# Performance work log

Hardware: AMD Instinct MI355X
Metric: run time of the kernel (lower is better)

The kernel has to match this reference:

```python
import jax, jax.numpy as jnp
import numpy as np

SMOOTH = 0.6


def setup_inputs() -> dict:
    key = jax.random.key(0)
    k1, k2 = jax.random.split(key)
    B, C, H, W = 32, 2, 1024, 1024
    outputs = jax.random.normal(k1, (B, C, H, W), dtype=jnp.float32)
    targets = jax.random.randint(k2, (B, H, W), 0, C, dtype=jnp.int64)
    return {"outputs": outputs, "targets": targets}


def reference(outputs, targets):
    B, C, H, W = outputs.shape
    # Per-sample bincount of class labels: counts [B, C]
    b_idx = jnp.arange(B)[:, None, None]
    counts = jnp.zeros((B, C), jnp.float32).at[b_idx, targets].add(1.0)
    # Instance weights: inverse-frequency, blended toward the per-sample mean
    weights = 1.0 - counts / counts.sum(axis=1, keepdims=True)
    weights = weights * (1.0 - SMOOTH) + weights.mean(axis=1, keepdims=True) * SMOOTH
    # Weighted cross-entropy per sample (F.cross_entropy mean reduction with
    # class weights divides by the sum of per-pixel weights)
    logp = jax.nn.log_softmax(outputs, axis=1)               # [B, C, H, W]
    nll = -jnp.take_along_axis(logp, targets[:, None], axis=1)[:, 0]  # [B, H, W]
    w_t = jnp.take_along_axis(weights, targets.reshape(B, -1), axis=1)
    w_t = w_t.reshape(B, H, W)                               # [B, H, W]
    per_sample = (w_t * nll).sum(axis=(1, 2)) / w_t.sum(axis=(1, 2))  # [B]
    return per_sample.mean()
```

## Files before the change

kernel.cpp:

```cpp
#include <hip/hip_runtime.h>

#define BB 32
#define HW (1024 * 1024)
#define BLOCKS_PER_SAMPLE 64
#define THREADS 256

__global__ __launch_bounds__(THREADS) void iwce_main(
    const float* __restrict__ outputs,
    const int* __restrict__ targets,
    float* __restrict__ s_all,
    float* __restrict__ s_one,
    unsigned int* __restrict__ c_one) {
    const int b = blockIdx.y;
    const int chunk = blockIdx.x;
    const int tid = threadIdx.x;

    const float* __restrict__ x0p = outputs + (size_t)b * 2 * HW;
    const float* __restrict__ x1p = x0p + HW;
    const int* __restrict__ tp = targets + (size_t)b * HW;

    const int pixelsPerBlock = HW / BLOCKS_PER_SAMPLE;
    const int base = chunk * pixelsPerBlock;
    const int iters = pixelsPerBlock / (THREADS * 4);

    float acc_all = 0.f;
    float acc_one = 0.f;
    unsigned int cnt_one = 0u;

#pragma unroll 4
    for (int j = 0; j < iters; ++j) {
        const int idx = base + (j * THREADS + tid) * 4;
        const float4 x0 = *reinterpret_cast<const float4*>(x0p + idx);
        const float4 x1 = *reinterpret_cast<const float4*>(x1p + idx);
        const int4 t = *reinterpret_cast<const int4*>(tp + idx);

        {
            const float a = x0.x, c = x1.x;
            const float m = fmaxf(a, c);
            const float nll = m + __logf(1.0f + __expf(-fabsf(a - c))) - (t.x ? c : a);
            acc_all += nll;
            if (t.x) { acc_one += nll; cnt_one++; }
        }
        {
            const float a = x0.y, c = x1.y;
            const float m = fmaxf(a, c);
            const float nll = m + __logf(1.0f + __expf(-fabsf(a - c))) - (t.y ? c : a);
            acc_all += nll;
            if (t.y) { acc_one += nll; cnt_one++; }
        }
        {
            const float a = x0.z, c = x1.z;
            const float m = fmaxf(a, c);
            const float nll = m + __logf(1.0f + __expf(-fabsf(a - c))) - (t.z ? c : a);
            acc_all += nll;
            if (t.z) { acc_one += nll; cnt_one++; }
        }
        {
            const float a = x0.w, c = x1.w;
            const float m = fmaxf(a, c);
            const float nll = m + __logf(1.0f + __expf(-fabsf(a - c))) - (t.w ? c : a);
            acc_all += nll;
            if (t.w) { acc_one += nll; cnt_one++; }
        }
    }

    const int lane = tid & 63;
    const int wid = tid >> 6;
#pragma unroll
    for (int off = 32; off; off >>= 1) {
        acc_all += __shfl_down(acc_all, off, 64);
        acc_one += __shfl_down(acc_one, off, 64);
        cnt_one += __shfl_down(cnt_one, off, 64);
    }
    __shared__ float sA[THREADS / 64], sO[THREADS / 64];
    __shared__ unsigned int sC[THREADS / 64];
    if (lane == 0) { sA[wid] = acc_all; sO[wid] = acc_one; sC[wid] = cnt_one; }
    __syncthreads();
    if (tid == 0) {
        float a = 0.f, o = 0.f; unsigned int c = 0u;
#pragma unroll
        for (int w = 0; w < THREADS / 64; ++w) { a += sA[w]; o += sO[w]; c += sC[w]; }
        atomicAdd(&s_all[b], a);
        atomicAdd(&s_one[b], o);
        atomicAdd(&c_one[b], c);
    }
}

__global__ __launch_bounds__(64) void iwce_final(
    const float* __restrict__ s_all,
    const float* __restrict__ s_one,
    const unsigned int* __restrict__ c_one,
    float* __restrict__ out) {
    const int lane = threadIdx.x;
    float v = 0.f;
    if (lane < BB) {
        const float sa = s_all[lane];
        const float s1 = s_one[lane];
        const float n1 = (float)c_one[lane];
        const float n0 = (float)HW - n1;
        const float invHW = 1.0f / (float)HW;
        const float w0 = (n1 * invHW) * 0.4f + 0.3f;
        const float w1 = (n0 * invHW) * 0.4f + 0.3f;
        const float num = w0 * (sa - s1) + w1 * s1;
        const float den = w0 * n0 + w1 * n1;
        v = num / den;
    }
#pragma unroll
    for (int off = 32; off; off >>= 1) v += __shfl_down(v, off, 64);
    if (lane == 0) out[0] = v * (1.0f / (float)BB);
}

extern "C" void kernel_launch(void* const* d_in, const int* in_sizes, int n_in,
                              void* d_out, int out_size, void* d_ws, size_t ws_size,
                              hipStream_t stream) {
    const float* outputs = (const float*)d_in[0];
    const int* targets = (const int*)d_in[1];
    float* out = (float*)d_out;

    float* s_all = (float*)d_ws;
    float* s_one = s_all + BB;
    unsigned int* c_one = (unsigned int*)(s_one + BB);

    hipMemsetAsync(d_ws, 0, (2 * BB) * sizeof(float) + BB * sizeof(unsigned int), stream);

    iwce_main<<<dim3(BLOCKS_PER_SAMPLE, BB), THREADS, 0, stream>>>(
        outputs, targets, s_all, s_one, c_one);
    iwce_final<<<1, 64, 0, stream>>>(s_all, s_one, c_one, out);
}
```

Baseline: 440.5 us.

## Use nontemporal loads, branchless accumulation, and per-block partials instead of atomics

Switches the streaming loads to nontemporal builtins, makes the per-pixel accumulation branchless, and replaces the global atomics with per-block partial sums that the final kernel reduces deterministically. This removes the memset launch and atomic contention. Counts are now accumulated as floats, which stays exact here because they never exceed 2^24.

```diff
diff --git a/kernel.cpp b/kernel.cpp
--- a/kernel.cpp
+++ b/kernel.cpp
@@ -3,17 +3,22 @@
 #define BB 32
 #define HW (1024 * 1024)
 #define BLOCKS_PER_SAMPLE 64
+#define NPART (BB * BLOCKS_PER_SAMPLE)
 #define THREADS 256
+
+typedef float v4f __attribute__((ext_vector_type(4)));
+typedef int v4i __attribute__((ext_vector_type(4)));
 
 __global__ __launch_bounds__(THREADS) void iwce_main(
     const float* __restrict__ outputs,
     const int* __restrict__ targets,
-    float* __restrict__ s_all,
-    float* __restrict__ s_one,
-    unsigned int* __restrict__ c_one) {
+    float* __restrict__ pA,
+    float* __restrict__ pO,
+    float* __restrict__ pC) {
     const int b = blockIdx.y;
     const int chunk = blockIdx.x;
     const int tid = threadIdx.x;
+    const int g = b * BLOCKS_PER_SAMPLE + chunk;
 
     const float* __restrict__ x0p = outputs + (size_t)b * 2 * HW;
     const float* __restrict__ x1p = x0p + HW;
@@ -25,89 +30,85 @@
 
     float acc_all = 0.f;
     float acc_one = 0.f;
-    unsigned int cnt_one = 0u;
+    int cnt_one = 0;
 
 #pragma unroll 4
     for (int j = 0; j < iters; ++j) {
         const int idx = base + (j * THREADS + tid) * 4;
-        const float4 x0 = *reinterpret_cast<const float4*>(x0p + idx);
-        const float4 x1 = *reinterpret_cast<const float4*>(x1p + idx);
-        const int4 t = *reinterpret_cast<const int4*>(tp + idx);
+        const v4f x0 = __builtin_nontemporal_load(reinterpret_cast<const v4f*>(x0p + idx));
+        const v4f x1 = __builtin_nontemporal_load(reinterpret_cast<const v4f*>(x1p + idx));
+        const v4i t = __builtin_nontemporal_load(reinterpret_cast<const v4i*>(tp + idx));
 
-        {
-            const float a = x0.x, c = x1.x;
+#pragma unroll
+        for (int k = 0; k < 4; ++k) {
+            const float a = x0[k], c = x1[k];
             const float m = fmaxf(a, c);
-            const float nll = m + __logf(1.0f + __expf(-fabsf(a - c))) - (t.x ? c : a);
+            const float nll = m + __logf(1.0f + __expf(-fabsf(a - c))) - (t[k] ? c : a);
             acc_all += nll;
-            if (t.x) { acc_one += nll; cnt_one++; }
-        }
-        {
-            const float a = x0.y, c = x1.y;
-            const float m = fmaxf(a, c);
-            const float nll = m + __logf(1.0f + __expf(-fabsf(a - c))) - (t.y ? c : a);
-            acc_all += nll;
-            if (t.y) { acc_one += nll; cnt_one++; }
-        }
-        {
-            const float a = x0.z, c = x1.z;
-            const float m = fmaxf(a, c);
-            const float nll = m + __logf(1.0f + __expf(-fabsf(a - c))) - (t.z ? c : a);
-            acc_all += nll;
-            if (t.z) { acc_one += nll; cnt_one++; }
-        }
-        {
-            const float a = x0.w, c = x1.w;
-            const float m = fmaxf(a, c);
-            const float nll = m + __logf(1.0f + __expf(-fabsf(a - c))) - (t.w ? c : a);
-            acc_all += nll;
-            if (t.w) { acc_one += nll; cnt_one++; }
+            acc_one += t[k] ? nll : 0.0f;
+            cnt_one += t[k];
         }
     }
 
     const int lane = tid & 63;
     const int wid = tid >> 6;
+    float acc_cnt = (float)cnt_one;
 #pragma unroll
     for (int off = 32; off; off >>= 1) {
         acc_all += __shfl_down(acc_all, off, 64);
         acc_one += __shfl_down(acc_one, off, 64);
-        cnt_one += __shfl_down(cnt_one, off, 64);
+        acc_cnt += __shfl_down(acc_cnt, off, 64);
     }
-    __shared__ float sA[THREADS / 64], sO[THREADS / 64];
-    __shared__ unsigned int sC[THREADS / 64];
-    if (lane == 0) { sA[wid] = acc_all; sO[wid] = acc_one; sC[wid] = cnt_one; }
+    __shared__ float sA[THREADS / 64], sO[THREADS / 64], sC[THREADS / 64];
+    if (lane == 0) { sA[wid] = acc_all; sO[wid] = acc_one; sC[wid] = acc_cnt; }
     __syncthreads();
     if (tid == 0) {
-        float a = 0.f, o = 0.f; unsigned int c = 0u;
+        float a = 0.f, o = 0.f, c = 0.f;
 #pragma unroll
         for (int w = 0; w < THREADS / 64; ++w) { a += sA[w]; o += sO[w]; c += sC[w]; }
-        atomicAdd(&s_all[b], a);
-        atomicAdd(&s_one[b], o);
-        atomicAdd(&c_one[b], c);
+        pA[g] = a; pO[g] = o; pC[g] = c;
     }
 }
 
-__global__ __launch_bounds__(64) void iwce_final(
-    const float* __restrict__ s_all,
-    const float* __restrict__ s_one,
-    const unsigned int* __restrict__ c_one,
+__global__ __launch_bounds__(1024) void iwce_final(
+    const float* __restrict__ pA,
+    const float* __restrict__ pO,
+    const float* __restrict__ pC,
     float* __restrict__ out) {
-    const int lane = threadIdx.x;
-    float v = 0.f;
-    if (lane < BB) {
-        const float sa = s_all[lane];
-        const float s1 = s_one[lane];
-        const float n1 = (float)c_one[lane];
-        const float n0 = (float)HW - n1;
-        const float invHW = 1.0f / (float)HW;
-        const float w0 = (n1 * invHW) * 0.4f + 0.3f;
-        const float w1 = (n0 * invHW) * 0.4f + 0.3f;
-        const float num = w0 * (sa - s1) + w1 * s1;
-        const float den = w0 * n0 + w1 * n1;
-        v = num / den;
+    const int tid = threadIdx.x;
+    const int wave = tid >> 6;
+    const int lane = tid & 63;
+    __shared__ float sv[BB];
+
+#pragma unroll
+    for (int s = 0; s < 2; ++s) {
+        const int b = wave + s * 16;
+        const int idx = b * BLOCKS_PER_SAMPLE + lane;
+        float a = pA[idx], o = pO[idx], c = pC[idx];
+#pragma unroll
+        for (int off = 32; off; off >>= 1) {
+            a += __shfl_down(a, off, 64);
+            o += __shfl_down(o, off, 64);
+            c += __shfl_down(c, off, 64);
+        }
+        if (lane == 0) {
+            const float n1 = c;
+            const float n0 = (float)HW - n1;
+            const float invHW = 1.0f / (float)HW;
+            const float w0 = (n1 * invHW) * 0.4f + 0.3f;
+            const float w1 = (n0 * invHW) * 0.4f + 0.3f;
+            const float num = w0 * (a - o) + w1 * o;
+            const float den = w0 * n0 + w1 * n1;
+            sv[b] = num / den;
+        }
     }
+    __syncthreads();
+    if (tid == 0) {
+        float s = 0.f;
 #pragma unroll
-    for (int off = 32; off; off >>= 1) v += __shfl_down(v, off, 64);
-    if (lane == 0) out[0] = v * (1.0f / (float)BB);
+        for (int b = 0; b < BB; ++b) s += sv[b];
+        out[0] = s * (1.0f / (float)BB);
+    }
 }
 
 extern "C" void kernel_launch(void* const* d_in, const int* in_sizes, int n_in,
@@ -117,13 +118,11 @@
     const int* targets = (const int*)d_in[1];
     float* out = (float*)d_out;
 
-    float* s_all = (float*)d_ws;
-    float* s_one = s_all + BB;
-    unsigned int* c_one = (unsigned int*)(s_one + BB);
-
-    hipMemsetAsync(d_ws, 0, (2 * BB) * sizeof(float) + BB * sizeof(unsigned int), stream);
+    float* pA = (float*)d_ws;
+    float* pO = pA + NPART;
+    float* pC = pO + NPART;
 
     iwce_main<<<dim3(BLOCKS_PER_SAMPLE, BB), THREADS, 0, stream>>>(
-        outputs, targets, s_all, s_one, c_one);
-    iwce_final<<<1, 64, 0, stream>>>(s_all, s_one, c_one, out);
+        outputs, targets, pA, pO, pC);
+    iwce_final<<<1, 1024, 0, stream>>>(pA, pO, pC, out);
 }
```

New measurement: 402.0 us. 8.7% less time.
